# Optimization experiments

Measured on AMD Instinct MI355X. Metric: run time of the kernel, lower is better.

Reference implementation:

```python
import jax, jax.numpy as jnp
import numpy as np
import math

V, L, D, H, S_MAX = 32000, 6, 768, 8, 256
HD = D // H
SCALE_FACTOR = 2  # attn_scale_factor in the original (TUPE-style)
POS_SCALING = float(HD * SCALE_FACTOR) ** (-0.5)
REL_BINS, MAX_DIST = 32, 128


def _rel_pos_bucket_np(rel, num_buckets=REL_BINS, max_distance=MAX_DIST):
    # bidirectional T5-style bucketing (faithful to relative_position_bucket)
    n = -rel
    num_buckets //= 2
    ret = (n < 0).astype(np.int64) * num_buckets
    n = np.abs(n)
    max_exact = num_buckets // 2
    is_small = n < max_exact
    val_if_large = max_exact + (
        np.log(np.maximum(n, 1).astype(np.float32) / max_exact)
        / math.log(max_distance / max_exact) * (num_buckets - max_exact)
    ).astype(np.int64)
    val_if_large = np.minimum(val_if_large, num_buckets - 1)
    ret += np.where(is_small, n, val_if_large)
    return ret


def _layernorm(x, g, b, eps=1e-5):
    mu = jnp.mean(x, axis=-1, keepdims=True)
    var = jnp.var(x, axis=-1, keepdims=True)
    return (x - mu) * jax.lax.rsqrt(var + eps) * g + b


def setup_inputs() -> dict:
    key = jax.random.key(0)
    ks = jax.random.split(key, 16)
    B, S = 32, 256
    init = lambda k, shape: (jax.random.normal(k, shape, jnp.float32) * 0.02)
    pos_idx = np.arange(S)
    rp = _rel_pos_bucket_np(pos_idx[None, :] - pos_idx[:, None])  # [S,S]
    return {
        "tokens": jax.random.randint(ks[0], (B, S), 0, V, dtype=jnp.int32),
        "embed_tokens": init(ks[1], (V, D)),
        "pos_emb": init(ks[2], (S_MAX + 1, D)),
        "pos_q_w": init(ks[3], (D, D)), "pos_q_b": jnp.zeros((D,), jnp.float32),
        "pos_k_w": init(ks[4], (D, D)), "pos_k_b": jnp.zeros((D,), jnp.float32),
        "pos_ln_g": jnp.ones((D,), jnp.float32), "pos_ln_b": jnp.zeros((D,), jnp.float32),
        "rel_bias_table": init(ks[5], (REL_BINS + 1, H)),
        "rp_bucket": jnp.asarray(rp, jnp.int32),
        "Wq": init(ks[6], (L, D, D)), "bq": jnp.zeros((L, D), jnp.float32),
        "Wk": init(ks[7], (L, D, D)), "bk": jnp.zeros((L, D), jnp.float32),
        "Wv": init(ks[8], (L, D, D)), "bv": jnp.zeros((L, D), jnp.float32),
        "Wo": init(ks[9], (L, D, D)), "bo": jnp.zeros((L, D), jnp.float32),
    }


def reference(tokens, embed_tokens, pos_emb, pos_q_w, pos_q_b, pos_k_w, pos_k_b,
              pos_ln_g, pos_ln_b, rel_bias_table, rp_bucket,
              Wq, bq, Wk, bk, Wv, bv, Wo, bo):
    B, S = tokens.shape
    # relative positional bias: bucket lookup -> [H,S,S]
    rel_bias = rel_bias_table[rp_bucket]            # [S,S,H]
    rel_bias = jnp.transpose(rel_bias, (2, 0, 1))   # [H,S,S]
    # absolute positional bias (TUPE): LN(pos) -> per-head q/k -> bmm
    w = _layernorm(pos_emb[:S], pos_ln_g, pos_ln_b)             # [S,D]
    pq = (w @ pos_q_w.T + pos_q_b).reshape(S, H, HD) * POS_SCALING
    pk = (w @ pos_k_w.T + pos_k_b).reshape(S, H, HD)
    abs_bias = jnp.einsum('ihd,jhd->hij', pq, pk)               # [H,S,S]
    bias = (abs_bias + rel_bias)[None]                          # [1,H,S,S]

    x = embed_tokens[tokens]                                    # [B,S,D]
    scale = float(HD * SCALE_FACTOR) ** (-0.5)
    for l in range(L):
        q = (x @ Wq[l].T + bq[l]).reshape(B, S, H, HD) * scale
        k = (x @ Wk[l].T + bk[l]).reshape(B, S, H, HD)
        v = (x @ Wv[l].T + bv[l]).reshape(B, S, H, HD)
        scores = jnp.einsum('bihd,bjhd->bhij', q, k) + bias     # [B,H,S,S]
        attn = jax.nn.softmax(scores, axis=-1)
        o = jnp.einsum('bhij,bjhd->bihd', attn, v).reshape(B, S, D)
        x = o @ Wo[l].T + bo[l]
    return x[:, 0, :]  # sentence rep [B,D]
```

## Files before the change

kernel.cpp:

```cpp
#include <hip/hip_runtime.h>
#include <hip/hip_bf16.h>
#include <math.h>

constexpr int SEQ = 256;
constexpr int DIM = 768;
constexpr int NH  = 8;
constexpr int HD  = 96;

typedef __attribute__((ext_vector_type(8))) short short8;
typedef __attribute__((ext_vector_type(4))) float f32x4;
using bf16 = __hip_bfloat16;

#define ASYNC_COPY16(gptr, lptr) \
  __builtin_amdgcn_global_load_lds((const __attribute__((address_space(1))) void*)(gptr), \
                                   (__attribute__((address_space(3))) void*)(lptr), 16, 0, 0)

__global__ __launch_bounds__(256) void gemm_kernel(
    const float* __restrict__ A, int lda, long aoz,
    const float* __restrict__ W, int ldw, long woz,
    const float* __restrict__ bias, long boz,
    float* __restrict__ C, int ldc, long coz,
    int M, int N, int K, float scale,
    const int* __restrict__ rp, const float* __restrict__ rtab)
{
    const int hz = blockIdx.z;
    A += (long)hz * aoz;
    W += (long)hz * woz;
    if (bias) bias += (long)hz * boz;
    C += (long)hz * coz;

    __shared__ float As[16][68];
    __shared__ float Ws[16][68];

    const int bm = blockIdx.y * 64;
    const int bn = blockIdx.x * 64;
    const int tid = threadIdx.x;
    const int tx = tid & 15;
    const int ty = tid >> 4;

    float acc[4][4] = {};

    for (int k0 = 0; k0 < K; k0 += 16) {
#pragma unroll
        for (int i = 0; i < 4; i++) {
            int idx = tid + i * 256;
            int r = idx >> 4, c = idx & 15;
            As[c][r] = A[(long)(bm + r) * lda + (k0 + c)];
            Ws[c][r] = W[(long)(bn + r) * ldw + (k0 + c)];
        }
        __syncthreads();
#pragma unroll
        for (int kk = 0; kk < 16; kk++) {
            const float4 a = *(const float4*)&As[kk][ty * 4];
            const float4 w = *(const float4*)&Ws[kk][tx * 4];
            acc[0][0] += a.x * w.x; acc[0][1] += a.x * w.y; acc[0][2] += a.x * w.z; acc[0][3] += a.x * w.w;
            acc[1][0] += a.y * w.x; acc[1][1] += a.y * w.y; acc[1][2] += a.y * w.z; acc[1][3] += a.y * w.w;
            acc[2][0] += a.z * w.x; acc[2][1] += a.z * w.y; acc[2][2] += a.z * w.z; acc[2][3] += a.z * w.w;
            acc[3][0] += a.w * w.x; acc[3][1] += a.w * w.y; acc[3][2] += a.w * w.z; acc[3][3] += a.w * w.w;
        }
        __syncthreads();
    }

    const int n0 = bn + tx * 4;
    float4 bv = make_float4(0.f, 0.f, 0.f, 0.f);
    if (bias) bv = *(const float4*)&bias[n0];
#pragma unroll
    for (int i = 0; i < 4; i++) {
        const int m = bm + ty * 4 + i;
        float4 r;
        if (rtab) {
            r.x = acc[i][0] * scale + rtab[rp[(n0 + 0) * 256 + m] * 8 + hz];
            r.y = acc[i][1] * scale + rtab[rp[(n0 + 1) * 256 + m] * 8 + hz];
            r.z = acc[i][2] * scale + rtab[rp[(n0 + 2) * 256 + m] * 8 + hz];
            r.w = acc[i][3] * scale + rtab[rp[(n0 + 3) * 256 + m] * 8 + hz];
        } else {
            r.x = (acc[i][0] + bv.x) * scale;
            r.y = (acc[i][1] + bv.y) * scale;
            r.z = (acc[i][2] + bv.z) * scale;
            r.w = (acc[i][3] + bv.w) * scale;
        }
        *(float4*)&C[(long)m * ldc + n0] = r;
    }
}

constexpr int RB_A = 10368;
constexpr int RB_B = RB_A + 3456;
constexpr int RB_C = RB_B + 54;
constexpr int RB_D = RB_C + 8192;
constexpr int RB_E = RB_D + 256;
constexpr int RB_F = RB_E + 1152;
constexpr int RB_G = RB_F + 2;

__global__ __launch_bounds__(256) void setup_mega_kernel(
    const int* __restrict__ tokens, const float* __restrict__ embed,
    const float* __restrict__ pos_emb,
    const float* __restrict__ pos_q_w, const float* __restrict__ pos_q_b,
    const float* __restrict__ pos_k_w, const float* __restrict__ pos_k_b,
    const float* __restrict__ pos_ln_g, const float* __restrict__ pos_ln_b,
    const float* __restrict__ Wq, const float* __restrict__ Wk,
    const float* __restrict__ Wv, const float* __restrict__ Wo,
    const float* __restrict__ bq, const float* __restrict__ bk,
    const float* __restrict__ bv,
    bf16* __restrict__ wqkv, bf16* __restrict__ woT, float* __restrict__ bqkv,
    bf16* __restrict__ xb, float* __restrict__ wln,
    float* __restrict__ wsW, float* __restrict__ wsB, float scale)
{
    const int bid = blockIdx.x, tid = threadIdx.x;

    if (bid < RB_A) {
        const long idx = (long)bid * 256 + tid;
        const long e = idx * 4;
        const int k = (int)(e % 768);
        const long nl = e / 768;
        const int n = (int)(nl % 2304);
        const int l = (int)(nl / 2304);
        const float* src;
        float sc = 1.f;
        if (n < 768)       { src = Wq + ((long)l * 768 + n) * 768; sc = scale; }
        else if (n < 1536) { src = Wk + ((long)l * 768 + (n - 768)) * 768; }
        else               { src = Wv + ((long)l * 768 + (n - 1536)) * 768; }
        const float4 v = *(const float4*)&src[k];
        bf16 tmp[4];
        tmp[0] = __float2bfloat16(v.x * sc);
        tmp[1] = __float2bfloat16(v.y * sc);
        tmp[2] = __float2bfloat16(v.z * sc);
        tmp[3] = __float2bfloat16(v.w * sc);
        *(uint2*)&wqkv[((long)l * 2304 + n) * 768 + k] = *(uint2*)tmp;
    } else if (bid < RB_B) {
        __shared__ float t[32][33];
        const int b2 = bid - RB_A;
        const int l = b2 / 576, r2 = b2 % 576;
        const int c0 = (r2 % 24) * 32, j0 = (r2 / 24) * 32;
        const int tx = tid & 31, ty = tid >> 5;
        const float* src = Wo + (long)l * 768 * 768;
#pragma unroll
        for (int rr = 0; rr < 32; rr += 8)
            t[ty + rr][tx] = src[(long)(c0 + ty + rr) * 768 + j0 + tx];
        __syncthreads();
        bf16* dst = woT + (long)l * 768 * 768;
#pragma unroll
        for (int rr = 0; rr < 32; rr += 8)
            dst[(long)(j0 + ty + rr) * 768 + c0 + tx] = __float2bfloat16(t[tx][ty + rr]);
    } else if (bid < RB_C) {
        const int idx = (bid - RB_B) * 256 + tid;
        if (idx < 6 * 2304) {
            const int n = idx % 2304, l = idx / 2304;
            float v;
            if (n < 768)       v = bq[l * 768 + n] * scale;
            else if (n < 1536) v = bk[l * 768 + (n - 768)];
            else               v = bv[l * 768 + (n - 1536)];
            bqkv[idx] = v;
        }
    } else if (bid < RB_D) {
        if (tid < 192) {
            const int t = bid - RB_C;
            const int tok = tokens[t];
            const float4 v = ((const float4*)(embed + (long)tok * DIM))[tid];
            bf16 tmp[4];
            tmp[0] = __float2bfloat16(v.x);
            tmp[1] = __float2bfloat16(v.y);
            tmp[2] = __float2bfloat16(v.z);
            tmp[3] = __float2bfloat16(v.w);
            *(uint2*)&xb[(long)t * DIM + tid * 4] = *(uint2*)tmp;
        }
    } else if (bid < RB_E) {
        __shared__ float buf[256];
        const int i = bid - RB_D;
        const float* row = pos_emb + (long)i * DIM;
        float v0 = row[tid], v1 = row[tid + 256], v2 = row[tid + 512];
        buf[tid] = v0 + v1 + v2;
        __syncthreads();
        for (int off = 128; off > 0; off >>= 1) {
            if (tid < off) buf[tid] += buf[tid + off];
            __syncthreads();
        }
        const float mean = buf[0] * (1.f / 768.f);
        __syncthreads();
        const float d0 = v0 - mean, d1 = v1 - mean, d2 = v2 - mean;
        buf[tid] = d0 * d0 + d1 * d1 + d2 * d2;
        __syncthreads();
        for (int off = 128; off > 0; off >>= 1) {
            if (tid < off) buf[tid] += buf[tid + off];
            __syncthreads();
        }
        const float rstd = rsqrtf(buf[0] * (1.f / 768.f) + 1e-5f);
        float* wr = wln + (long)i * DIM;
        wr[tid]       = d0 * rstd * pos_ln_g[tid]       + pos_ln_b[tid];
        wr[tid + 256] = d1 * rstd * pos_ln_g[tid + 256] + pos_ln_b[tid + 256];
        wr[tid + 512] = d2 * rstd * pos_ln_g[tid + 512] + pos_ln_b[tid + 512];
    } else if (bid < RB_F) {
        const long idx = (long)(bid - RB_E) * 256 + tid;
        const long e = idx * 4;
        const float4 v = (e < 589824) ? *(const float4*)&pos_q_w[e]
                                      : *(const float4*)&pos_k_w[e - 589824];
        *(float4*)&wsW[e] = v;
    } else {
        const int idx = (bid - RB_F) * 256 + tid;
        wsB[idx] = (idx < 768) ? pos_q_b[idx] : pos_k_b[idx - 768];
    }
}

__global__ __launch_bounds__(256) void fused_bias_kernel(
    const bf16* __restrict__ wqkv, const float* __restrict__ bo,
    const float* __restrict__ bqkv, float* __restrict__ bf_)
{
    const int l = blockIdx.y;
    const int lane = threadIdx.x & 63, wave = threadIdx.x >> 6;
    const int nloc = wave * 8 + (lane >> 3);
    const int seg = lane & 7;
    const int n = blockIdx.x * 32 + nloc;
    const bf16* wrow = wqkv + ((long)(l + 1) * 2304 + n) * 768 + seg * 96;
    const float* bsrc = bo + (long)l * 768 + seg * 96;
    float s = 0.f;
#pragma unroll
    for (int c8 = 0; c8 < 12; c8++) {
        const short8 w8 = *(const short8*)&wrow[c8 * 8];
#pragma unroll
        for (int e = 0; e < 8; e++) {
            bf16 b;
            *(short*)&b = w8[e];
            s += __bfloat162float(b) * bsrc[c8 * 8 + e];
        }
    }
    s += __shfl_xor(s, 1);
    s += __shfl_xor(s, 2);
    s += __shfl_xor(s, 4);
    if (seg == 0) bf_[l * 2304 + n] = s + bqkv[(l + 1) * 2304 + n];
}

#define GEMM_PREF(AS, BS, KB)                                                 \
  {                                                                           \
    _Pragma("unroll")                                                         \
    for (int i = 0; i < 2; i++) {                                             \
      const int u = tid + i * 512;                                            \
      const int r = u >> 3, c = u & 7;                                        \
      const int ca = c ^ (r & 7);                                             \
      ASYNC_COPY16(A + (bm + r) * (long)K + (KB) + ca * 8, &AS[u * 8]);       \
      ASYNC_COPY16(B + (bn + r) * (long)K + (KB) + ca * 8, &BS[u * 8]);       \
    }                                                                         \
  }

#define GEMM_COMPUTE(AS, BS)                                                  \
  {                                                                           \
    _Pragma("unroll")                                                         \
    for (int ks = 0; ks < 2; ks++) {                                          \
      const int cc = ks * 4 + quad;                                           \
      short8 af[4], bfr[2];                                                   \
      _Pragma("unroll")                                                       \
      for (int t = 0; t < 4; t++) {                                           \
        const int ra = wm * 64 + t * 16 + col;                                \
        af[t] = *(const short8*)&AS[ra * 64 + ((cc ^ (ra & 7)) * 8)];         \
      }                                                                       \
      _Pragma("unroll")                                                       \
      for (int t = 0; t < 2; t++) {                                           \
        const int rb = wn * 32 + t * 16 + col;                                \
        bfr[t] = *(const short8*)&BS[rb * 64 + ((cc ^ (rb & 7)) * 8)];        \
      }                                                                       \
      _Pragma("unroll")                                                       \
      for (int tm = 0; tm < 4; tm++)                                          \
        _Pragma("unroll")                                                     \
        for (int tn = 0; tn < 2; tn++)                                        \
          acc[tm][tn] = __builtin_amdgcn_mfma_f32_16x16x32_bf16(af[tm], bfr[tn], acc[tm][tn], 0, 0, 0); \
    }                                                                         \
  }

__global__ __launch_bounds__(512, 4) void gemm_bf16_kernel(
    const bf16* __restrict__ A, const bf16* __restrict__ B,
    const float* __restrict__ bias,
    bf16* __restrict__ Cb, bf16* __restrict__ vTout,
    int N, int K, int swz, long az, long bz, long cz, int skipQ)
{
    __shared__ bf16 As0[128 * 64];
    __shared__ bf16 Bs0[128 * 64];
    __shared__ bf16 As1[128 * 64];
    __shared__ bf16 Bs1[128 * 64];

    A += (long)blockIdx.z * az;
    B += (long)blockIdx.z * bz;
    if (Cb) Cb += (long)blockIdx.z * cz;

    const int tid = threadIdx.x;
    const int lane = tid & 63, wave = tid >> 6;
    const int wm = wave & 1, wn = wave >> 1;

    int bmt, bnt;
    if (swz) {
        const int id = blockIdx.x + gridDim.x * blockIdx.y;
        const int xcd = id & 7, loc = id >> 3;
        bmt = xcd * 8 + (loc & 7);
        bnt = loc >> 3;
    } else {
        bmt = blockIdx.y;
        bnt = blockIdx.x;
    }
    if (skipQ && bnt < 6 && (bmt & 1)) return;

    const long bm = (long)bmt * 128, bn = (long)bnt * 128;
    const int col = lane & 15, quad = lane >> 4;

    f32x4 acc[4][2] = {};

    GEMM_PREF(As0, Bs0, 0);
    for (int kk = 0; kk < K; kk += 128) {
        __syncthreads();
        GEMM_PREF(As1, Bs1, kk + 64);
        GEMM_COMPUTE(As0, Bs0);
        __syncthreads();
        if (kk + 128 < K) GEMM_PREF(As0, Bs0, kk + 128);
        GEMM_COMPUTE(As1, Bs1);
    }

    const bool toVT = (vTout != nullptr) && (bn >= 1536);

    if (toVT) {
        __syncthreads();
        bf16* tb = (wave < 4 ? As0 : Bs0) + (wave & 3) * 2048;
#pragma unroll
        for (int tn = 0; tn < 2; tn++) {
            const int nl = tn * 16 + col;
            const float bvv = bias[bn + wn * 32 + nl];
#pragma unroll
            for (int tm = 0; tm < 4; tm++) {
                const int mc = tm * 4 + quad;
                bf16 t4[4];
#pragma unroll
                for (int r = 0; r < 4; r++)
                    t4[r] = __float2bfloat16(acc[tm][tn][r] + bvv);
                *(uint2*)&tb[(nl * 16 + (mc ^ (nl & 15))) * 4] = *(uint2*)t4;
            }
        }
        const int b_  = (int)((bm + wm * 64) >> 8);
        const int s0  = (int)((bm + wm * 64) & 255);
        const long nb = bn + wn * 32 - 1536;
#pragma unroll
        for (int it2 = 0; it2 < 8; it2++) {
            const int nl = it2 * 4 + quad;
            const uint2 v = *(const uint2*)&tb[(nl * 16 + (col ^ (nl & 15))) * 4];
            *(uint2*)&vTout[((long)b_ * 768 + nb + nl) * 256 + s0 + col * 4] = v;
        }
    } else {
#pragma unroll
        for (int tn = 0; tn < 2; tn++) {
            const long n = bn + wn * 32 + tn * 16 + col;
            const float bvv = bias ? bias[n] : 0.f;
#pragma unroll
            for (int tm = 0; tm < 4; tm++) {
                const long m0 = bm + wm * 64 + tm * 16 + quad * 4;
#pragma unroll
                for (int r = 0; r < 4; r++)
                    Cb[(m0 + r) * N + n] = __float2bfloat16(acc[tm][tn][r] + bvv);
            }
        }
    }
}

#define PREF_K(DST, JC)                                                      \
  { _Pragma("unroll")                                                        \
    for (int i = 0; i < 4; i++) {                                            \
      const int u = tid + i * 256;                                           \
      const int r = u >> 4, pp = u & 15;                                     \
      const int c = pp ^ (r & 15);                                           \
      ASYNC_COPY16(kbase + ((JC) * 64 + r) * 2304 + c * 8, &DST[u * 8]);     \
    } }

#define PREF_V(DST, KC)                                                      \
  { _Pragma("unroll")                                                        \
    for (int i = 0; i < 3; i++) {                                            \
      const int u = tid + i * 256;                                           \
      const int r = u >> 3, pp = u & 7;                                      \
      const int c = pp ^ (r & 7);                                            \
      ASYNC_COPY16(vbase + r * 256 + (KC) * 64 + c * 8, &DST[u * 8]);        \
    } }

#define SCORE(BUF, JC)                                                       \
  { _Pragma("unroll")                                                        \
    for (int ks = 0; ks < 3; ks++) {                                         \
      _Pragma("unroll")                                                      \
      for (int jt2 = 0; jt2 < 4; jt2++) {                                    \
        const int row = jt2 * 16 + col;                                      \
        const int c = ks * 4 + quad;                                         \
        const short8 bk_ = *(const short8*)&BUF[row * 128 + ((c ^ (row & 15)) * 8)]; \
        accS[(JC) * 4 + jt2] = __builtin_amdgcn_mfma_f32_16x16x32_bf16(aq[ks], bk_, accS[(JC) * 4 + jt2], 0, 0, 0); \
      } } }

#define PV(BUF, KC)                                                          \
  { _Pragma("unroll")                                                        \
    for (int k2 = 0; k2 < 2; k2++) {                                         \
      const short8 ap = *(const short8*)&Ps[(wave * 16 + col) * PS + (KC) * 64 + k2 * 32 + quad * 8]; \
      _Pragma("unroll")                                                      \
      for (int nt = 0; nt < 6; nt++) {                                       \
        const int row = nt * 16 + col;                                       \
        const int c = k2 * 4 + quad;                                         \
        const short8 bv_ = *(const short8*)&BUF[row * 64 + ((c ^ (row & 7)) * 8)]; \
        accO[nt] = __builtin_amdgcn_mfma_f32_16x16x32_bf16(ap, bv_, accO[nt], 0, 0, 0); \
      } } }

__global__ __launch_bounds__(256) void attn_mfma_kernel(
    const bf16* __restrict__ qkv, const bf16* __restrict__ vT,
    const float* __restrict__ biasT, bf16* __restrict__ o)
{
    constexpr int PS = 264;
    __shared__ bf16 Ps[64 * PS];
    __shared__ bf16 KV0[64 * 128];
    __shared__ bf16 KV1[64 * 128];

    const int blk = blockIdx.x;
    const int b  = blk & 31;
    const int h  = (blk >> 5) & 7;
    const int it = blk >> 8;
    const int i0 = it * 64;
    const int tid = threadIdx.x, lane = tid & 63, wave = tid >> 6;
    const int col = lane & 15, quad = lane >> 4;
    const long rowbase = (long)b * SEQ;

    const bf16* kbase = qkv + rowbase * 2304 + 768 + h * 96;
    const bf16* vbase = vT + ((long)b * 768 + h * 96) * 256;

    PREF_K(KV0, 0);

    short8 aq[3];
    {
        const bf16* qrow = qkv + (rowbase + i0 + wave * 16 + col) * 2304 + h * 96;
#pragma unroll
        for (int ks = 0; ks < 3; ks++)
            aq[ks] = *(const short8*)&qrow[ks * 32 + quad * 8];
    }

    f32x4 accS[16] = {};
    __syncthreads();
    PREF_K(KV1, 1);
    SCORE(KV0, 0);
    __syncthreads();
    PREF_K(KV0, 2);
    SCORE(KV1, 1);
    __syncthreads();
    PREF_K(KV1, 3);
    SCORE(KV0, 2);
    __syncthreads();
    PREF_V(KV0, 0);
    SCORE(KV1, 3);

    const float* bbT = biasT + (long)h * SEQ * SEQ + i0 + wave * 16 + quad * 4;
#pragma unroll
    for (int jt = 0; jt < 16; jt++) {
        const float4 bv4 = *(const float4*)&bbT[(jt * 16 + col) * SEQ];
        accS[jt][0] += bv4.x;
        accS[jt][1] += bv4.y;
        accS[jt][2] += bv4.z;
        accS[jt][3] += bv4.w;
    }

#pragma unroll
    for (int r = 0; r < 4; r++) {
        float m = accS[0][r];
#pragma unroll
        for (int jt = 1; jt < 16; jt++) m = fmaxf(m, accS[jt][r]);
        for (int d = 1; d < 16; d <<= 1) m = fmaxf(m, __shfl_xor(m, d));
        float s = 0.f;
#pragma unroll
        for (int jt = 0; jt < 16; jt++) {
            const float e = __expf(accS[jt][r] - m);
            accS[jt][r] = e;
            s += e;
        }
        for (int d = 1; d < 16; d <<= 1) s += __shfl_xor(s, d);
        const float inv = 1.f / s;
        const int prow = wave * 16 + quad * 4 + r;
#pragma unroll
        for (int jt = 0; jt < 16; jt++)
            Ps[prow * PS + jt * 16 + col] = __float2bfloat16(accS[jt][r] * inv);
    }

    f32x4 accO[6] = {};
    __syncthreads();
    PREF_V(KV1, 1);
    PV(KV0, 0);
    __syncthreads();
    PREF_V(KV0, 2);
    PV(KV1, 1);
    __syncthreads();
    PREF_V(KV1, 3);
    PV(KV0, 2);
    __syncthreads();
    PV(KV1, 3);

#pragma unroll
    for (int nt = 0; nt < 6; nt++)
#pragma unroll
        for (int r = 0; r < 4; r++) {
            const long m = rowbase + i0 + wave * 16 + quad * 4 + r;
            o[m * DIM + h * 96 + nt * 16 + col] = __float2bfloat16(accO[nt][r]);
        }
}

__global__ __launch_bounds__(256) void final_out_kernel(
    const bf16* __restrict__ ob, const float* __restrict__ Wo5,
    const float* __restrict__ bo5, float* __restrict__ out)
{
    __shared__ float os[768];
    const int b = blockIdx.y, ng = blockIdx.x, tid = threadIdx.x;
    const bf16* orow = ob + (long)b * 256 * 768;
    for (int i = tid; i < 768; i += 256) os[i] = __bfloat162float(orow[i]);
    __syncthreads();

    const int n = ng * 32 + (tid >> 3);
    const int seg = tid & 7;
    const float* wrow = Wo5 + (long)n * 768 + seg * 96;
    const float* xs = &os[seg * 96];
    float s = 0.f;
#pragma unroll
    for (int k = 0; k < 96; k += 4) {
        const float4 w = *(const float4*)&wrow[k];
        s += xs[k] * w.x + xs[k + 1] * w.y + xs[k + 2] * w.z + xs[k + 3] * w.w;
    }
    s += __shfl_xor(s, 1);
    s += __shfl_xor(s, 2);
    s += __shfl_xor(s, 4);
    if (seg == 0) out[b * 768 + n] = s + bo5[n];
}

extern "C" void kernel_launch(void* const* d_in, const int* in_sizes, int n_in,
                              void* d_out, int out_size, void* d_ws, size_t ws_size,
                              hipStream_t stream)
{
    const int*   tokens   = (const int*)d_in[0];
    const float* embed    = (const float*)d_in[1];
    const float* pos_emb  = (const float*)d_in[2];
    const float* pos_q_w  = (const float*)d_in[3];
    const float* pos_q_b  = (const float*)d_in[4];
    const float* pos_k_w  = (const float*)d_in[5];
    const float* pos_k_b  = (const float*)d_in[6];
    const float* pos_ln_g = (const float*)d_in[7];
    const float* pos_ln_b = (const float*)d_in[8];
    const float* rel_tab  = (const float*)d_in[9];
    const int*   rp       = (const int*)d_in[10];
    const float* Wq = (const float*)d_in[11];
    const float* bq = (const float*)d_in[12];
    const float* Wk = (const float*)d_in[13];
    const float* bk = (const float*)d_in[14];
    const float* Wv = (const float*)d_in[15];
    const float* bv = (const float*)d_in[16];
    const float* Wo = (const float*)d_in[17];
    const float* bo = (const float*)d_in[18];
    float* out = (float*)d_out;

    char* p = (char*)d_ws;
    auto alloc = [&](size_t bytes) -> char* {
        char* r = p;
        p += (bytes + 255) & ~(size_t)255;
        return r;
    };
    const long NT = 32L * SEQ;

    float* biasT = (float*)alloc(8L * SEQ * SEQ * 4);
    float* wln   = (float*)alloc((long)SEQ * DIM * 4);
    float* pqk   = (float*)alloc(2L * SEQ * DIM * 4);
    float* wsW   = (float*)alloc(2L * 768 * 768 * 4);
    float* wsB   = (float*)alloc(2L * 768 * 4);
    bf16*  xb    = (bf16*) alloc(NT * DIM * 2);
    bf16*  qkv   = (bf16*) alloc(NT * 2304 * 2);
    bf16*  vT    = (bf16*) alloc(NT * DIM * 2);
    bf16*  ob    = (bf16*) alloc(NT * DIM * 2);
    bf16*  wqkv  = (bf16*) alloc(6L * 2304 * 768 * 2);
    bf16*  woT   = (bf16*) alloc(6L * 768 * 768 * 2);
    bf16*  wf    = (bf16*) alloc(5L * 2304 * 768 * 2);
    float* bqkv  = (float*)alloc(6L * 2304 * 4);
    float* bfus  = (float*)alloc(5L * 2304 * 4);

    const float SCALE = 0.07216878364870322f;

    setup_mega_kernel<<<RB_G, 256, 0, stream>>>(
        tokens, embed, pos_emb, pos_q_w, pos_q_b, pos_k_w, pos_k_b,
        pos_ln_g, pos_ln_b, Wq, Wk, Wv, Wo, bq, bk, bv,
        wqkv, woT, bqkv, xb, wln, wsW, wsB, SCALE);

    gemm_bf16_kernel<<<dim3(6, 18, 5), 512, 0, stream>>>(
        wqkv + 2304L * 768, woT, nullptr, wf, nullptr, 768, 768, 0,
        2304L * 768, 768L * 768, 2304L * 768, 0);
    fused_bias_kernel<<<dim3(72, 5), 256, 0, stream>>>(wqkv, bo, bqkv, bfus);

    gemm_kernel<<<dim3(12, 4, 2), 256, 0, stream>>>(
        wln, DIM, 0, wsW, DIM, 768L * 768, wsB, 768,
        pqk, DIM, (long)SEQ * DIM, SEQ, DIM, DIM, 1.0f, nullptr, nullptr);
    gemm_kernel<<<dim3(4, 4, NH), 256, 0, stream>>>(
        pqk + (long)SEQ * DIM, DIM, HD, pqk, DIM, HD, nullptr, 0,
        biasT, SEQ, (long)SEQ * SEQ, SEQ, SEQ, HD, SCALE, rp, rel_tab);

    gemm_bf16_kernel<<<dim3(18, 64, 1), 512, 0, stream>>>(xb, wqkv, bqkv, qkv, vT, 2304, 768, 1, 0, 0, 0, 0);
    for (int l = 0; l < 5; l++) {
        attn_mfma_kernel<<<1024, 256, 0, stream>>>(qkv, vT, biasT, ob);
        gemm_bf16_kernel<<<dim3(18, 64, 1), 512, 0, stream>>>(
            ob, wf + (long)l * 2304 * 768, bfus + (long)l * 2304, qkv, vT, 2304, 768, 1, 0, 0, 0,
            (l == 4) ? 1 : 0);
    }
    attn_mfma_kernel<<<256, 256, 0, stream>>>(qkv, vT, biasT, ob);
    final_out_kernel<<<dim3(24, 32), 256, 0, stream>>>(ob, Wo + 5L * 768 * 768, bo + 5L * 768, out);
}
```

Before: 672.0 us.

## Move positional projection to bf16 MFMA GEMM and store bias in bf16

The positional q/k projection moves from the fp32 SIMT GEMM to the bf16 MFMA GEMM, which gains an fp32 output path with per-z bias. The LN output and weights are stored in bf16 to feed it. The combined attention bias is stored in bf16, halving the bias reads in every attention launch. The token embedding gather is repacked so all threads in a block work instead of only 192. The cost is lower precision in the positional bias.

Result: faster. 640.0 us (-4.8%).

```diff
diff --git a/kernel.cpp b/kernel.cpp
--- a/kernel.cpp
+++ b/kernel.cpp
@@ -19,7 +19,7 @@
     const float* __restrict__ A, int lda, long aoz,
     const float* __restrict__ W, int ldw, long woz,
     const float* __restrict__ bias, long boz,
-    float* __restrict__ C, int ldc, long coz,
+    bf16* __restrict__ C, int ldc, long coz,
     int M, int N, int K, float scale,
     const int* __restrict__ rp, const float* __restrict__ rtab)
 {
@@ -79,14 +79,19 @@
             r.z = (acc[i][2] + bv.z) * scale;
             r.w = (acc[i][3] + bv.w) * scale;
         }
-        *(float4*)&C[(long)m * ldc + n0] = r;
+        bf16 t4[4];
+        t4[0] = __float2bfloat16(r.x);
+        t4[1] = __float2bfloat16(r.y);
+        t4[2] = __float2bfloat16(r.z);
+        t4[3] = __float2bfloat16(r.w);
+        *(uint2*)&C[(long)m * ldc + n0] = *(uint2*)t4;
     }
 }
 
 constexpr int RB_A = 10368;
 constexpr int RB_B = RB_A + 3456;
 constexpr int RB_C = RB_B + 54;
-constexpr int RB_D = RB_C + 8192;
+constexpr int RB_D = RB_C + 6144;
 constexpr int RB_E = RB_D + 256;
 constexpr int RB_F = RB_E + 1152;
 constexpr int RB_G = RB_F + 2;
@@ -102,8 +107,8 @@
     const float* __restrict__ bq, const float* __restrict__ bk,
     const float* __restrict__ bv,
     bf16* __restrict__ wqkv, bf16* __restrict__ woT, float* __restrict__ bqkv,
-    bf16* __restrict__ xb, float* __restrict__ wln,
-    float* __restrict__ wsW, float* __restrict__ wsB, float scale)
+    bf16* __restrict__ xb, bf16* __restrict__ wln,
+    bf16* __restrict__ wsW, float* __restrict__ wsB, float scale)
 {
     const int bid = blockIdx.x, tid = threadIdx.x;
 
@@ -152,17 +157,17 @@
             bqkv[idx] = v;
         }
     } else if (bid < RB_D) {
-        if (tid < 192) {
-            const int t = bid - RB_C;
-            const int tok = tokens[t];
-            const float4 v = ((const float4*)(embed + (long)tok * DIM))[tid];
-            bf16 tmp[4];
-            tmp[0] = __float2bfloat16(v.x);
-            tmp[1] = __float2bfloat16(v.y);
-            tmp[2] = __float2bfloat16(v.z);
-            tmp[3] = __float2bfloat16(v.w);
-            *(uint2*)&xb[(long)t * DIM + tid * 4] = *(uint2*)tmp;
-        }
+        const int idx = (bid - RB_C) * 256 + tid;
+        const int t = idx / 192;
+        const int d = idx - t * 192;
+        const int tok = tokens[t];
+        const float4 v = ((const float4*)(embed + (long)tok * DIM))[d];
+        bf16 tmp[4];
+        tmp[0] = __float2bfloat16(v.x);
+        tmp[1] = __float2bfloat16(v.y);
+        tmp[2] = __float2bfloat16(v.z);
+        tmp[3] = __float2bfloat16(v.w);
+        *(uint2*)&xb[(long)t * DIM + d * 4] = *(uint2*)tmp;
     } else if (bid < RB_E) {
         __shared__ float buf[256];
         const int i = bid - RB_D;
@@ -184,16 +189,21 @@
             __syncthreads();
         }
         const float rstd = rsqrtf(buf[0] * (1.f / 768.f) + 1e-5f);
-        float* wr = wln + (long)i * DIM;
-        wr[tid]       = d0 * rstd * pos_ln_g[tid]       + pos_ln_b[tid];
-        wr[tid + 256] = d1 * rstd * pos_ln_g[tid + 256] + pos_ln_b[tid + 256];
-        wr[tid + 512] = d2 * rstd * pos_ln_g[tid + 512] + pos_ln_b[tid + 512];
+        bf16* wr = wln + (long)i * DIM;
+        wr[tid]       = __float2bfloat16(d0 * rstd * pos_ln_g[tid]       + pos_ln_b[tid]);
+        wr[tid + 256] = __float2bfloat16(d1 * rstd * pos_ln_g[tid + 256] + pos_ln_b[tid + 256]);
+        wr[tid + 512] = __float2bfloat16(d2 * rstd * pos_ln_g[tid + 512] + pos_ln_b[tid + 512]);
     } else if (bid < RB_F) {
         const long idx = (long)(bid - RB_E) * 256 + tid;
         const long e = idx * 4;
         const float4 v = (e < 589824) ? *(const float4*)&pos_q_w[e]
                                       : *(const float4*)&pos_k_w[e - 589824];
-        *(float4*)&wsW[e] = v;
+        bf16 tmp[4];
+        tmp[0] = __float2bfloat16(v.x);
+        tmp[1] = __float2bfloat16(v.y);
+        tmp[2] = __float2bfloat16(v.z);
+        tmp[3] = __float2bfloat16(v.w);
+        *(uint2*)&wsW[e] = *(uint2*)tmp;
     } else {
         const int idx = (bid - RB_F) * 256 + tid;
         wsB[idx] = (idx < 768) ? pos_q_b[idx] : pos_k_b[idx - 768];
@@ -267,8 +277,8 @@
 __global__ __launch_bounds__(512, 4) void gemm_bf16_kernel(
     const bf16* __restrict__ A, const bf16* __restrict__ B,
     const float* __restrict__ bias,
-    bf16* __restrict__ Cb, bf16* __restrict__ vTout,
-    int N, int K, int swz, long az, long bz, long cz, int skipQ)
+    bf16* __restrict__ Cb, bf16* __restrict__ vTout, float* __restrict__ Cf,
+    int N, int K, int swz, long az, long bz, long cz, long biasz, int skipQ)
 {
     __shared__ bf16 As0[128 * 64];
     __shared__ bf16 Bs0[128 * 64];
@@ -278,6 +288,8 @@
     A += (long)blockIdx.z * az;
     B += (long)blockIdx.z * bz;
     if (Cb) Cb += (long)blockIdx.z * cz;
+    if (Cf) Cf += (long)blockIdx.z * cz;
+    if (bias) bias += (long)blockIdx.z * biasz;
 
     const int tid = threadIdx.x;
     const int lane = tid & 63, wave = tid >> 6;
@@ -337,6 +349,19 @@
             const int nl = it2 * 4 + quad;
             const uint2 v = *(const uint2*)&tb[(nl * 16 + (col ^ (nl & 15))) * 4];
             *(uint2*)&vTout[((long)b_ * 768 + nb + nl) * 256 + s0 + col * 4] = v;
+        }
+    } else if (Cf) {
+#pragma unroll
+        for (int tn = 0; tn < 2; tn++) {
+            const long n = bn + wn * 32 + tn * 16 + col;
+            const float bvv = bias ? bias[n] : 0.f;
+#pragma unroll
+            for (int tm = 0; tm < 4; tm++) {
+                const long m0 = bm + wm * 64 + tm * 16 + quad * 4;
+#pragma unroll
+                for (int r = 0; r < 4; r++)
+                    Cf[(m0 + r) * N + n] = acc[tm][tn][r] + bvv;
+            }
         }
     } else {
 #pragma unroll
@@ -397,7 +422,7 @@
 
 __global__ __launch_bounds__(256) void attn_mfma_kernel(
     const bf16* __restrict__ qkv, const bf16* __restrict__ vT,
-    const float* __restrict__ biasT, bf16* __restrict__ o)
+    const bf16* __restrict__ biasT, bf16* __restrict__ o)
 {
     constexpr int PS = 264;
     __shared__ bf16 Ps[64 * PS];
@@ -440,14 +465,15 @@
     PREF_V(KV0, 0);
     SCORE(KV1, 3);
 
-    const float* bbT = biasT + (long)h * SEQ * SEQ + i0 + wave * 16 + quad * 4;
+    const bf16* bbT = biasT + (long)h * SEQ * SEQ + i0 + wave * 16 + quad * 4;
 #pragma unroll
     for (int jt = 0; jt < 16; jt++) {
-        const float4 bv4 = *(const float4*)&bbT[(jt * 16 + col) * SEQ];
-        accS[jt][0] += bv4.x;
-        accS[jt][1] += bv4.y;
-        accS[jt][2] += bv4.z;
-        accS[jt][3] += bv4.w;
+        bf16 b4[4];
+        *(uint2*)b4 = *(const uint2*)&bbT[(long)(jt * 16 + col) * SEQ];
+        accS[jt][0] += __bfloat162float(b4[0]);
+        accS[jt][1] += __bfloat162float(b4[1]);
+        accS[jt][2] += __bfloat162float(b4[2]);
+        accS[jt][3] += __bfloat162float(b4[3]);
     }
 
 #pragma unroll
@@ -552,10 +578,10 @@
     };
     const long NT = 32L * SEQ;
 
-    float* biasT = (float*)alloc(8L * SEQ * SEQ * 4);
-    float* wln   = (float*)alloc((long)SEQ * DIM * 4);
+    bf16*  biasT = (bf16*) alloc(8L * SEQ * SEQ * 2);
+    bf16*  wlnb  = (bf16*) alloc((long)SEQ * DIM * 2);
     float* pqk   = (float*)alloc(2L * SEQ * DIM * 4);
-    float* wsW   = (float*)alloc(2L * 768 * 768 * 4);
+    bf16*  wsWb  = (bf16*) alloc(2L * 768 * 768 * 2);
     float* wsB   = (float*)alloc(2L * 768 * 4);
     bf16*  xb    = (bf16*) alloc(NT * DIM * 2);
     bf16*  qkv   = (bf16*) alloc(NT * 2304 * 2);
@@ -572,26 +598,27 @@
     setup_mega_kernel<<<RB_G, 256, 0, stream>>>(
         tokens, embed, pos_emb, pos_q_w, pos_q_b, pos_k_w, pos_k_b,
         pos_ln_g, pos_ln_b, Wq, Wk, Wv, Wo, bq, bk, bv,
-        wqkv, woT, bqkv, xb, wln, wsW, wsB, SCALE);
+        wqkv, woT, bqkv, xb, wlnb, wsWb, wsB, SCALE);
 
     gemm_bf16_kernel<<<dim3(6, 18, 5), 512, 0, stream>>>(
-        wqkv + 2304L * 768, woT, nullptr, wf, nullptr, 768, 768, 0,
-        2304L * 768, 768L * 768, 2304L * 768, 0);
+        wqkv + 2304L * 768, woT, nullptr, wf, nullptr, nullptr, 768, 768, 0,
+        2304L * 768, 768L * 768, 2304L * 768, 0, 0);
     fused_bias_kernel<<<dim3(72, 5), 256, 0, stream>>>(wqkv, bo, bqkv, bfus);
 
-    gemm_kernel<<<dim3(12, 4, 2), 256, 0, stream>>>(
-        wln, DIM, 0, wsW, DIM, 768L * 768, wsB, 768,
-        pqk, DIM, (long)SEQ * DIM, SEQ, DIM, DIM, 1.0f, nullptr, nullptr);
+    gemm_bf16_kernel<<<dim3(6, 2, 2), 512, 0, stream>>>(
+        wlnb, wsWb, wsB, nullptr, nullptr, pqk, 768, 768, 0,
+        0, 768L * 768, (long)SEQ * DIM, 768, 0);
     gemm_kernel<<<dim3(4, 4, NH), 256, 0, stream>>>(
         pqk + (long)SEQ * DIM, DIM, HD, pqk, DIM, HD, nullptr, 0,
         biasT, SEQ, (long)SEQ * SEQ, SEQ, SEQ, HD, SCALE, rp, rel_tab);
 
-    gemm_bf16_kernel<<<dim3(18, 64, 1), 512, 0, stream>>>(xb, wqkv, bqkv, qkv, vT, 2304, 768, 1, 0, 0, 0, 0);
+    gemm_bf16_kernel<<<dim3(18, 64, 1), 512, 0, stream>>>(
+        xb, wqkv, bqkv, qkv, vT, nullptr, 2304, 768, 1, 0, 0, 0, 0, 0);
     for (int l = 0; l < 5; l++) {
         attn_mfma_kernel<<<1024, 256, 0, stream>>>(qkv, vT, biasT, ob);
         gemm_bf16_kernel<<<dim3(18, 64, 1), 512, 0, stream>>>(
-            ob, wf + (long)l * 2304 * 768, bfus + (long)l * 2304, qkv, vT, 2304, 768, 1, 0, 0, 0,
-            (l == 4) ? 1 : 0);
+            ob, wf + (long)l * 2304 * 768, bfus + (long)l * 2304, qkv, vT, nullptr,
+            2304, 768, 1, 0, 0, 0, 0, (l == 4) ? 1 : 0);
     }
     attn_mfma_kernel<<<256, 256, 0, stream>>>(qkv, vT, biasT, ob);
     final_out_kernel<<<dim3(24, 32), 256, 0, stream>>>(ob, Wo + 5L * 768 * 768, bo + 5L * 768, out);
```
